# Kernel tuning notes

Measured on AMD Instinct MI355X. Metric: run time of the kernel, lower is better.

Reference implementation:

```python
import jax, jax.numpy as jnp
import numpy as np
import math

B, S, D, H = 2, 2048, 1024, 16
DK = D // H

def setup_inputs() -> dict:
    key = jax.random.key(0)
    ks = jax.random.split(key, 12)
    scale = 0.02
    return {
        "q": jax.random.normal(ks[0], (B, S, D), jnp.float32),
        "k": jax.random.normal(ks[1], (B, S, D), jnp.float32),
        "v": jax.random.normal(ks[2], (B, S, D), jnp.float32),
        "mask": jnp.ones((B, S), jnp.int32),
        "Wq": jax.random.normal(ks[3], (D, D), jnp.float32) * scale,
        "bq": jnp.zeros((D,), jnp.float32),
        "Wk": jax.random.normal(ks[4], (D, D), jnp.float32) * scale,
        "bk": jnp.zeros((D,), jnp.float32),
        "Wv": jax.random.normal(ks[5], (D, D), jnp.float32) * scale,
        "bv": jnp.zeros((D,), jnp.float32),
        "Wo": jax.random.normal(ks[6], (D, D), jnp.float32) * scale,
        "bo": jnp.zeros((D,), jnp.float32),
    }

def _split_heads(x):
    b, s, d = x.shape
    return x.reshape(b, s, H, DK).transpose(0, 2, 1, 3)  # [b,h,s,dk]

def reference(q, k, v, mask, Wq, bq, Wk, bk, Wv, bv, Wo, bo):
    Q = _split_heads(q @ Wq.T + bq)
    K = _split_heads(k @ Wk.T + bk)
    V = _split_heads(v @ Wv.T + bv)
    scores = jnp.einsum('bhqd,bhkd->bhqk', Q, K) / math.sqrt(DK)
    # mask dim==2 path: [b,s] -> [b,1,1,s]
    m = mask[:, None, None, :]
    scores = jnp.where(m == 0, jnp.float32(-1e9), scores)
    attn = jax.nn.softmax(scores, axis=-1)  # dropout is identity in eval
    out = jnp.einsum('bhqk,bhkd->bhqd', attn, V)
    out = out.transpose(0, 2, 1, 3).reshape(q.shape[0], q.shape[1], D)
    return out @ Wo.T + bo
```

## Files before the change

### kernel.cpp

```cpp
#include <hip/hip_runtime.h>
#include <math.h>

#define D_MODEL 1024
#define NHEAD   16
#define DKH     64
#define SEQ     2048
#define BATCH   2
#define TOK     (BATCH*SEQ)

typedef short s16x8 __attribute__((ext_vector_type(8)));
typedef float f32x4 __attribute__((ext_vector_type(4)));
typedef float f32x16 __attribute__((ext_vector_type(16)));
typedef unsigned short ushort_t;

__device__ inline unsigned short f2bf(float f) {
    union { float f; unsigned u; } v; v.f = f;
    unsigned r = v.u + 0x7FFFu + ((v.u >> 16) & 1u);
    return (unsigned short)(r >> 16);
}
__device__ inline float bf2f(ushort_t h) {
    union { unsigned u; float f; } v; v.u = (unsigned)h << 16;
    return v.f;
}
__device__ inline unsigned cvt_pk_bf16(float a, float b) {
    unsigned r;
    asm("v_cvt_pk_bf16_f32 %0, %1, %2" : "=v"(r) : "v"(a), "v"(b));
    return r;
}
__device__ inline void gload16(const void* g, void* l) {
    __builtin_amdgcn_global_load_lds(
        (const __attribute__((address_space(1))) void*)g,
        (__attribute__((address_space(3))) void*)l, 16, 0, 0);
}
__device__ inline f32x16 zero16() {
    f32x16 v;
#pragma unroll
    for (int i = 0; i < 16; ++i) v[i] = 0.f;
    return v;
}

__global__ __launch_bounds__(256) void convert_all(
    const float* __restrict__ q, const float* __restrict__ k,
    const float* __restrict__ v,
    const float* __restrict__ Wq, const float* __restrict__ Wk,
    const float* __restrict__ Wv, const float* __restrict__ Wo,
    const int* __restrict__ mask,
    ushort_t* __restrict__ qb, ushort_t* __restrict__ kb,
    ushort_t* __restrict__ vb,
    ushort_t* __restrict__ Wqb, ushort_t* __restrict__ Wkb,
    ushort_t* __restrict__ Wvb, ushort_t* __restrict__ Wohi,
    ushort_t* __restrict__ Wolo, float* __restrict__ mb)
{
    const int ACT4 = TOK * D_MODEL / 4;
    const int W4   = D_MODEL * D_MODEL / 4;
    const int total = 3 * ACT4 + 4 * W4 + TOK / 4;
    for (int u = blockIdx.x * 256 + threadIdx.x; u < total; u += gridDim.x * 256) {
        if (u < 3 * ACT4) {
            int which = u / ACT4, off = u - which * ACT4;
            const float* src = which == 0 ? q : which == 1 ? k : v;
            ushort_t*    dst = which == 0 ? qb : which == 1 ? kb : vb;
            float4 f = ((const float4*)src)[off];
            uint2 o;
            o.x = cvt_pk_bf16(f.x, f.y);
            o.y = cvt_pk_bf16(f.z, f.w);
            ((uint2*)dst)[off] = o;
        } else if (u < 3 * ACT4 + 3 * W4) {
            int uu = u - 3 * ACT4;
            int which = uu / W4, off = uu - which * W4;
            const float* src = which == 0 ? Wq : which == 1 ? Wk : Wv;
            ushort_t*    dst = which == 0 ? Wqb : which == 1 ? Wkb : Wvb;
            float4 f = ((const float4*)src)[off];
            uint2 o;
            o.x = cvt_pk_bf16(f.x, f.y);
            o.y = cvt_pk_bf16(f.z, f.w);
            ((uint2*)dst)[off] = o;
        } else if (u < 3 * ACT4 + 4 * W4) {
            int off = u - (3 * ACT4 + 3 * W4);
            float4 f = ((const float4*)Wo)[off];
            ushort_t h0 = f2bf(f.x), h1 = f2bf(f.y), h2 = f2bf(f.z), h3 = f2bf(f.w);
            uint2 hw;
            hw.x = (unsigned)h0 | ((unsigned)h1 << 16);
            hw.y = (unsigned)h2 | ((unsigned)h3 << 16);
            ((uint2*)Wohi)[off] = hw;
            uint2 lw;
            lw.x = cvt_pk_bf16(f.x - bf2f(h0), f.y - bf2f(h1));
            lw.y = cvt_pk_bf16(f.z - bf2f(h2), f.w - bf2f(h3));
            ((uint2*)Wolo)[off] = lw;
        } else {
            int off = u - (3 * ACT4 + 4 * W4);
            int4 m = ((const int4*)mask)[off];
            float4 f;
            f.x = m.x ? 0.f : -1e9f;
            f.y = m.y ? 0.f : -1e9f;
            f.z = m.z ? 0.f : -1e9f;
            f.w = m.w ? 0.f : -1e9f;
            ((float4*)mb)[off] = f;
        }
    }
}

__global__ __launch_bounds__(256) void gemm_qkv(
    const ushort_t* __restrict__ qb, const ushort_t* __restrict__ kb,
    const ushort_t* __restrict__ vb,
    const ushort_t* __restrict__ Wqb, const ushort_t* __restrict__ Wkb,
    const ushort_t* __restrict__ Wvb,
    const float* __restrict__ bqp, const float* __restrict__ bkp,
    const float* __restrict__ bvp,
    ushort_t* __restrict__ Qb, ushort_t* __restrict__ Kb,
    ushort_t* __restrict__ Vtb)
{
    __shared__ __align__(16) char pool[64 * 136 * 2];
    ushort_t* As = (ushort_t*)pool;
    ushort_t* Ws = As + 128 * 32;

    const int z = blockIdx.z;
    const ushort_t* Ain  = z == 0 ? qb : z == 1 ? kb : vb;
    const ushort_t* Wptr = z == 0 ? Wqb : z == 1 ? Wkb : Wvb;
    const float*    bias = z == 0 ? bqp : z == 1 ? bkp : bvp;

    const int hwid = blockIdx.x + 8 * blockIdx.y;
    const int work = (hwid & 7) * 32 + (hwid >> 3);
    const int m0 = (work >> 3) * 128;
    const int n0 = (work & 7) * 128;

    const int t = threadIdx.x;
    const int w = t >> 6, lane = t & 63, l15 = lane & 15, l4 = lane >> 4;
    const int wr = w >> 1, wc = w & 1;

    f32x4 acc[4][4];
#pragma unroll
    for (int m = 0; m < 4; ++m)
#pragma unroll
        for (int n = 0; n < 4; ++n) acc[m][n] = (f32x4){0.f, 0.f, 0.f, 0.f};

    const ushort_t* Ag = Ain  + (size_t)(m0 + (t >> 2)) * D_MODEL + (t & 3) * 8;
    const ushort_t* Wg = Wptr + (size_t)(n0 + (t >> 2)) * D_MODEL + (t & 3) * 8;
    ushort_t* AsW = As + w * 512;
    ushort_t* WsW = Ws + w * 512;

    for (int k0 = 0; k0 < D_MODEL; k0 += 32) {
        __syncthreads();
        gload16(Ag + k0, AsW);
        gload16(Ag + (size_t)64 * D_MODEL + k0, AsW + 2048);
        gload16(Wg + k0, WsW);
        gload16(Wg + (size_t)64 * D_MODEL + k0, WsW + 2048);
        __syncthreads();

        s16x8 af[4], bfr[4];
#pragma unroll
        for (int m = 0; m < 4; ++m)
            af[m] = *(const s16x8*)&As[(wr * 64 + m * 16 + l15) * 32 + l4 * 8];
#pragma unroll
        for (int n = 0; n < 4; ++n)
            bfr[n] = *(const s16x8*)&Ws[(wc * 64 + n * 16 + l15) * 32 + l4 * 8];
#pragma unroll
        for (int m = 0; m < 4; ++m)
#pragma unroll
            for (int n = 0; n < 4; ++n)
                acc[m][n] = __builtin_amdgcn_mfma_f32_16x16x32_bf16(af[m], bfr[n], acc[m][n], 0, 0, 0);
    }

    if (z == 2) {
        ushort_t* Ct = (ushort_t*)pool;
        const int h0 = n0 >> 6;
        const int bb = m0 >> 11;
        const int s0 = m0 & (SEQ - 1);
#pragma unroll
        for (int hh = 0; hh < 2; ++hh) {
            __syncthreads();
            if (wc == hh) {
#pragma unroll
                for (int n = 0; n < 4; ++n) {
                    const int nl = n * 16 + l15;
                    const float bv = bias[n0 + hh * 64 + nl];
#pragma unroll
                    for (int m = 0; m < 4; ++m) {
                        const int ml = wr * 64 + m * 16 + l4 * 4;
#pragma unroll
                        for (int r = 0; r < 4; ++r)
                            Ct[nl * 136 + ml + r] = f2bf(acc[m][n][r] + bv);
                    }
                }
            }
            __syncthreads();
            const int dl = t >> 2;
            ushort_t* dst = Vtb + (((size_t)bb * NHEAD + h0 + hh) * DKH + dl) * SEQ + s0;
#pragma unroll
            for (int c = 0; c < 4; ++c) {
                int chk = (t & 3) + c * 4;
                *(uint4*)&dst[chk * 8] = *(const uint4*)&Ct[dl * 136 + chk * 8];
            }
        }
    } else {
        ushort_t* Cout = z == 0 ? Qb : Kb;
#pragma unroll
        for (int n = 0; n < 4; ++n) {
            const int col = n0 + wc * 64 + n * 16 + l15;
            const float bv = bias[col];
#pragma unroll
            for (int m = 0; m < 4; ++m) {
                const int row = m0 + wr * 64 + m * 16 + l4 * 4;
#pragma unroll
                for (int r = 0; r < 4; ++r)
                    Cout[(size_t)(row + r) * D_MODEL + col] = f2bf(acc[m][n][r] + bv);
            }
        }
    }
}

__global__ __launch_bounds__(256) void gemm_out(
    const ushort_t* __restrict__ Ain, const ushort_t* __restrict__ Wptr,
    const ushort_t* __restrict__ W2ptr, const float* __restrict__ bias,
    float* __restrict__ Cout)
{
    __shared__ ushort_t As[128 * 32];
    __shared__ ushort_t Ws[64 * 32];
    __shared__ ushort_t Ws2[64 * 32];

    const int hwid = blockIdx.x + 16 * blockIdx.y;
    const int work = (hwid & 7) * 64 + (hwid >> 3);
    const int m0 = (work >> 4) * 128;
    const int n0 = (work & 15) * 64;

    const int t = threadIdx.x;
    const int w = t >> 6, lane = t & 63, l15 = lane & 15, l4 = lane >> 4;
    const int wr = w >> 1, wc = w & 1;

    f32x4 acc[4][2];
#pragma unroll
    for (int m = 0; m < 4; ++m)
#pragma unroll
        for (int n = 0; n < 2; ++n) acc[m][n] = (f32x4){0.f, 0.f, 0.f, 0.f};

    const ushort_t* Ag  = Ain   + (size_t)(m0 + (t >> 2)) * D_MODEL + (t & 3) * 8;
    const ushort_t* Wg  = Wptr  + (size_t)(n0 + (t >> 2)) * D_MODEL + (t & 3) * 8;
    const ushort_t* W2g = W2ptr + (size_t)(n0 + (t >> 2)) * D_MODEL + (t & 3) * 8;
    ushort_t* AsW = As + w * 512;
    ushort_t* WsW = Ws + w * 512;
    ushort_t* Ws2W = Ws2 + w * 512;

    for (int k0 = 0; k0 < D_MODEL; k0 += 32) {
        __syncthreads();
        gload16(Ag + k0, AsW);
        gload16(Ag + (size_t)64 * D_MODEL + k0, AsW + 2048);
        gload16(Wg + k0, WsW);
        gload16(W2g + k0, Ws2W);
        __syncthreads();

        s16x8 af[4], bfr[2], bfr2[2];
#pragma unroll
        for (int m = 0; m < 4; ++m)
            af[m] = *(const s16x8*)&As[(wr * 64 + m * 16 + l15) * 32 + l4 * 8];
#pragma unroll
        for (int n = 0; n < 2; ++n) {
            bfr[n]  = *(const s16x8*)&Ws[(wc * 32 + n * 16 + l15) * 32 + l4 * 8];
            bfr2[n] = *(const s16x8*)&Ws2[(wc * 32 + n * 16 + l15) * 32 + l4 * 8];
        }
#pragma unroll
        for (int m = 0; m < 4; ++m)
#pragma unroll
            for (int n = 0; n < 2; ++n) {
                acc[m][n] = __builtin_amdgcn_mfma_f32_16x16x32_bf16(af[m], bfr[n],  acc[m][n], 0, 0, 0);
                acc[m][n] = __builtin_amdgcn_mfma_f32_16x16x32_bf16(af[m], bfr2[n], acc[m][n], 0, 0, 0);
            }
    }

#pragma unroll
    for (int n = 0; n < 2; ++n) {
        const int col = n0 + wc * 32 + n * 16 + l15;
        const float bv = bias[col];
#pragma unroll
        for (int m = 0; m < 4; ++m) {
            const int row = m0 + wr * 64 + m * 16 + l4 * 4;
#pragma unroll
            for (int r = 0; r < 4; ++r)
                Cout[(size_t)(row + r) * D_MODEL + col] = acc[m][n][r] + bv;
        }
    }
}

__global__ __launch_bounds__(256) void flash5(
    const ushort_t* __restrict__ Q, const ushort_t* __restrict__ K,
    const ushort_t* __restrict__ Vt, const float* __restrict__ mb,
    ushort_t* __restrict__ Ctx)
{
    __shared__ ushort_t Ks[64 * 72];
    __shared__ ushort_t Vs[64 * 72];
    __shared__ ushort_t Ps[128 * 72];

    const int t = threadIdx.x;
    const int w = t >> 6, lane = t & 63;
    const int l31 = lane & 31, lh = lane >> 5;
    const int q0 = blockIdx.y * 128;
    const int bh = blockIdx.x, b = bh >> 4, h = bh & 15;

    s16x8 qf[4];
    {
        const ushort_t* qp = Q + ((size_t)b * SEQ + q0 + w * 32 + l31) * D_MODEL + h * DKH + lh * 8;
#pragma unroll
        for (int ks = 0; ks < 4; ++ks)
            qf[ks] = *(const s16x8*)(qp + ks * 16);
    }

    f32x16 oacc0 = zero16(), oacc1 = zero16();
    float lpart[16];
#pragma unroll
    for (int i = 0; i < 16; ++i) lpart[i] = 0.f;

    const int ch   = t & 7;
    const int row0 = t >> 3;
    const ushort_t* Kg = K  + ((size_t)b * SEQ) * D_MODEL + h * DKH + ch * 8;
    const ushort_t* Vg = Vt + ((size_t)bh * DKH) * SEQ + ch * 8;

    uint4 kr0 = *(const uint4*)&Kg[(size_t)row0 * D_MODEL];
    uint4 kr1 = *(const uint4*)&Kg[(size_t)(row0 + 32) * D_MODEL];
    uint4 vr0 = *(const uint4*)&Vg[(size_t)row0 * SEQ];
    uint4 vr1 = *(const uint4*)&Vg[(size_t)(row0 + 32) * SEQ];

    const float CSC = 0.18033688011112042f;
    const float* mbp = mb + b * SEQ;
    const int prow = w * 32;

    for (int k0 = 0; k0 < SEQ; k0 += 64) {
        __syncthreads();
        *(uint4*)&Ks[row0 * 72 + ch * 8]        = kr0;
        *(uint4*)&Ks[(row0 + 32) * 72 + ch * 8] = kr1;
        *(uint4*)&Vs[row0 * 72 + ch * 8]        = vr0;
        *(uint4*)&Vs[(row0 + 32) * 72 + ch * 8] = vr1;
        __syncthreads();
        if (k0 + 64 < SEQ) {
            kr0 = *(const uint4*)&Kg[(size_t)(k0 + 64 + row0) * D_MODEL];
            kr1 = *(const uint4*)&Kg[(size_t)(k0 + 64 + row0 + 32) * D_MODEL];
            vr0 = *(const uint4*)&Vg[(size_t)row0 * SEQ + k0 + 64];
            vr1 = *(const uint4*)&Vg[(size_t)(row0 + 32) * SEQ + k0 + 64];
        }
        const float mb0 = mbp[k0 + l31];
        const float mb1 = mbp[k0 + 32 + l31];

        f32x16 sacc0 = zero16(), sacc1 = zero16();
        __builtin_amdgcn_s_setprio(1);
#pragma unroll
        for (int ks = 0; ks < 4; ++ks) {
            s16x8 kf0 = *(const s16x8*)&Ks[(l31)      * 72 + ks * 16 + lh * 8];
            s16x8 kf1 = *(const s16x8*)&Ks[(32 + l31) * 72 + ks * 16 + lh * 8];
            sacc0 = __builtin_amdgcn_mfma_f32_32x32x16_bf16(qf[ks], kf0, sacc0, 0, 0, 0);
            sacc1 = __builtin_amdgcn_mfma_f32_32x32x16_bf16(qf[ks], kf1, sacc1, 0, 0, 0);
        }
        __builtin_amdgcn_s_setprio(0);

#pragma unroll
        for (int rp = 0; rp < 8; ++rp) {
            const int r0 = 2 * rp;
            const int rowb = (r0 & 3) + 8 * (r0 >> 2) + 4 * lh;
            float p0 = __builtin_amdgcn_exp2f(fmaf(sacc0[r0],     CSC, mb0));
            float p1 = __builtin_amdgcn_exp2f(fmaf(sacc0[r0 + 1], CSC, mb0));
            float p2 = __builtin_amdgcn_exp2f(fmaf(sacc1[r0],     CSC, mb1));
            float p3 = __builtin_amdgcn_exp2f(fmaf(sacc1[r0 + 1], CSC, mb1));
            lpart[r0]     += p0 + p2;
            lpart[r0 + 1] += p1 + p3;
            unsigned ua = cvt_pk_bf16(p0, p1);
            unsigned ub = cvt_pk_bf16(p2, p3);
            int base0 = (prow + rowb) * 72 + l31;
            Ps[base0]           = (ushort_t)ua;
            Ps[base0 + 72]      = (ushort_t)(ua >> 16);
            Ps[base0 + 32]      = (ushort_t)ub;
            Ps[base0 + 72 + 32] = (ushort_t)(ub >> 16);
        }
        __builtin_amdgcn_sched_barrier(0);

        __builtin_amdgcn_s_setprio(1);
#pragma unroll
        for (int ks = 0; ks < 4; ++ks) {
            s16x8 pa  = *(const s16x8*)&Ps[(prow + l31) * 72 + ks * 16 + lh * 8];
            s16x8 vf0 = *(const s16x8*)&Vs[(l31)      * 72 + ks * 16 + lh * 8];
            s16x8 vf1 = *(const s16x8*)&Vs[(32 + l31) * 72 + ks * 16 + lh * 8];
            oacc0 = __builtin_amdgcn_mfma_f32_32x32x16_bf16(pa, vf0, oacc0, 0, 0, 0);
            oacc1 = __builtin_amdgcn_mfma_f32_32x32x16_bf16(pa, vf1, oacc1, 0, 0, 0);
        }
        __builtin_amdgcn_s_setprio(0);
    }

#pragma unroll
    for (int rg = 0; rg < 16; ++rg) {
        lpart[rg] += __shfl_xor(lpart[rg], 1);
        lpart[rg] += __shfl_xor(lpart[rg], 2);
        lpart[rg] += __shfl_xor(lpart[rg], 4);
        lpart[rg] += __shfl_xor(lpart[rg], 8);
        lpart[rg] += __shfl_xor(lpart[rg], 16);
    }
    const size_t obase = ((size_t)b * SEQ + q0 + w * 32) * D_MODEL + h * DKH + l31;
#pragma unroll
    for (int rg = 0; rg < 16; ++rg) {
        const int qrow = (rg & 3) + 8 * (rg >> 2) + 4 * lh;
        const float inv = 1.f / lpart[rg];
        Ctx[obase + (size_t)qrow * D_MODEL]      = f2bf(oacc0[rg] * inv);
        Ctx[obase + (size_t)qrow * D_MODEL + 32] = f2bf(oacc1[rg] * inv);
    }
}

extern "C" void kernel_launch(void* const* d_in, const int* in_sizes, int n_in,
                              void* d_out, int out_size, void* d_ws, size_t ws_size,
                              hipStream_t stream) {
    const float* q    = (const float*)d_in[0];
    const float* k    = (const float*)d_in[1];
    const float* v    = (const float*)d_in[2];
    const int*   mask = (const int*)  d_in[3];
    const float* Wq   = (const float*)d_in[4];
    const float* bq   = (const float*)d_in[5];
    const float* Wk   = (const float*)d_in[6];
    const float* bk   = (const float*)d_in[7];
    const float* Wv   = (const float*)d_in[8];
    const float* bv   = (const float*)d_in[9];
    const float* Wo   = (const float*)d_in[10];
    const float* bo   = (const float*)d_in[11];
    float* out = (float*)d_out;

    char* ws = (char*)d_ws;
    ushort_t* Wqb  = (ushort_t*)(ws);
    ushort_t* Wkb  = (ushort_t*)(ws + ( 2u << 20));
    ushort_t* Wvb  = (ushort_t*)(ws + ( 4u << 20));
    ushort_t* Wohi = (ushort_t*)(ws + ( 6u << 20));
    ushort_t* Wolo = (ushort_t*)(ws + ( 8u << 20));
    float*    mb   = (float*)   (ws + (10u << 20));
    ushort_t* qb   = (ushort_t*)(ws + (12u << 20));
    ushort_t* kb   = (ushort_t*)(ws + (20u << 20));
    ushort_t* vb   = (ushort_t*)(ws + (28u << 20));
    ushort_t* Qb   = (ushort_t*)(ws + (36u << 20));
    ushort_t* Kb   = (ushort_t*)(ws + (44u << 20));
    ushort_t* Vtb  = (ushort_t*)(ws + (52u << 20));
    ushort_t* Ctx  = qb;

    convert_all<<<2048, 256, 0, stream>>>(q, k, v, Wq, Wk, Wv, Wo, mask,
                                          qb, kb, vb, Wqb, Wkb, Wvb,
                                          Wohi, Wolo, mb);

    dim3 qkvgrid(D_MODEL / 128, TOK / 128, 3);
    gemm_qkv<<<qkvgrid, 256, 0, stream>>>(qb, kb, vb, Wqb, Wkb, Wvb,
                                          bq, bk, bv, Qb, Kb, Vtb);

    dim3 agrid(BATCH * NHEAD, SEQ / 128);
    flash5<<<agrid, 256, 0, stream>>>(Qb, Kb, Vtb, mb, Ctx);

    dim3 ogrid(D_MODEL / 64, TOK / 128);
    gemm_out<<<ogrid, 256, 0, stream>>>(Ctx, Wohi, Wolo, bo, out);
}
```

Baseline: 150.6 us.

## Split attention over two key halves and add a combine kernel

The flash attention kernel now runs a third grid dimension that splits the key sequence into two halves. Each half writes unnormalized bf16 partial outputs and per-row softmax denominators to workspace, and a new combine kernel sums the two partials and normalizes them. This doubles the number of attention blocks, aiming to fill the GPU better than the previous 512-block grid. The cost is an extra launch, extra global traffic for two partial output buffers, and an added bf16 rounding of the unnormalized accumulators.

```diff
diff --git a/kernel.cpp b/kernel.cpp
--- a/kernel.cpp
+++ b/kernel.cpp
@@ -279,10 +279,11 @@
     }
 }
 
-__global__ __launch_bounds__(256) void flash5(
+__global__ __launch_bounds__(256) void flash8(
     const ushort_t* __restrict__ Q, const ushort_t* __restrict__ K,
     const ushort_t* __restrict__ Vt, const float* __restrict__ mb,
-    ushort_t* __restrict__ Ctx)
+    ushort_t* __restrict__ O0, ushort_t* __restrict__ O1,
+    float* __restrict__ Lp)
 {
     __shared__ ushort_t Ks[64 * 72];
     __shared__ ushort_t Vs[64 * 72];
@@ -293,6 +294,8 @@
     const int l31 = lane & 31, lh = lane >> 5;
     const int q0 = blockIdx.y * 128;
     const int bh = blockIdx.x, b = bh >> 4, h = bh & 15;
+    const int z  = blockIdx.z;
+    const int kbase = z * (SEQ / 2);
 
     s16x8 qf[4];
     {
@@ -312,23 +315,24 @@
     const ushort_t* Kg = K  + ((size_t)b * SEQ) * D_MODEL + h * DKH + ch * 8;
     const ushort_t* Vg = Vt + ((size_t)bh * DKH) * SEQ + ch * 8;
 
-    uint4 kr0 = *(const uint4*)&Kg[(size_t)row0 * D_MODEL];
-    uint4 kr1 = *(const uint4*)&Kg[(size_t)(row0 + 32) * D_MODEL];
-    uint4 vr0 = *(const uint4*)&Vg[(size_t)row0 * SEQ];
-    uint4 vr1 = *(const uint4*)&Vg[(size_t)(row0 + 32) * SEQ];
+    uint4 kr0 = *(const uint4*)&Kg[(size_t)(kbase + row0) * D_MODEL];
+    uint4 kr1 = *(const uint4*)&Kg[(size_t)(kbase + row0 + 32) * D_MODEL];
+    uint4 vr0 = *(const uint4*)&Vg[(size_t)row0 * SEQ + kbase];
+    uint4 vr1 = *(const uint4*)&Vg[(size_t)(row0 + 32) * SEQ + kbase];
 
     const float CSC = 0.18033688011112042f;
     const float* mbp = mb + b * SEQ;
     const int prow = w * 32;
 
-    for (int k0 = 0; k0 < SEQ; k0 += 64) {
+    const int kend = kbase + SEQ / 2;
+    for (int k0 = kbase; k0 < kend; k0 += 64) {
         __syncthreads();
         *(uint4*)&Ks[row0 * 72 + ch * 8]        = kr0;
         *(uint4*)&Ks[(row0 + 32) * 72 + ch * 8] = kr1;
         *(uint4*)&Vs[row0 * 72 + ch * 8]        = vr0;
         *(uint4*)&Vs[(row0 + 32) * 72 + ch * 8] = vr1;
         __syncthreads();
-        if (k0 + 64 < SEQ) {
+        if (k0 + 64 < kend) {
             kr0 = *(const uint4*)&Kg[(size_t)(k0 + 64 + row0) * D_MODEL];
             kr1 = *(const uint4*)&Kg[(size_t)(k0 + 64 + row0 + 32) * D_MODEL];
             vr0 = *(const uint4*)&Vg[(size_t)row0 * SEQ + k0 + 64];
@@ -388,14 +392,43 @@
         lpart[rg] += __shfl_xor(lpart[rg], 8);
         lpart[rg] += __shfl_xor(lpart[rg], 16);
     }
+    ushort_t* Op = z == 0 ? O0 : O1;
+    float* lp = Lp + (size_t)z * TOK * NHEAD;
     const size_t obase = ((size_t)b * SEQ + q0 + w * 32) * D_MODEL + h * DKH + l31;
 #pragma unroll
     for (int rg = 0; rg < 16; ++rg) {
         const int qrow = (rg & 3) + 8 * (rg >> 2) + 4 * lh;
-        const float inv = 1.f / lpart[rg];
-        Ctx[obase + (size_t)qrow * D_MODEL]      = f2bf(oacc0[rg] * inv);
-        Ctx[obase + (size_t)qrow * D_MODEL + 32] = f2bf(oacc1[rg] * inv);
-    }
+        Op[obase + (size_t)qrow * D_MODEL]      = f2bf(oacc0[rg]);
+        Op[obase + (size_t)qrow * D_MODEL + 32] = f2bf(oacc1[rg]);
+        if (l31 == 0)
+            lp[((size_t)b * SEQ + q0 + w * 32 + qrow) * NHEAD + h] = lpart[rg];
+    }
+}
+
+__global__ __launch_bounds__(256) void combine(
+    const ushort_t* __restrict__ O0, const ushort_t* __restrict__ O1,
+    const float* __restrict__ Lp, ushort_t* __restrict__ Ctx)
+{
+    const int idx = blockIdx.x * 256 + threadIdx.x;
+    const int e   = idx * 8;
+    const int row = e >> 10;
+    const int h   = (e & (D_MODEL - 1)) >> 6;
+    const float l0 = Lp[(size_t)row * NHEAD + h];
+    const float l1 = Lp[(size_t)TOK * NHEAD + (size_t)row * NHEAD + h];
+    const float inv = 1.f / (l0 + l1);
+    uint4 a = ((const uint4*)O0)[idx];
+    uint4 c = ((const uint4*)O1)[idx];
+    const unsigned* au = (const unsigned*)&a;
+    const unsigned* cu = (const unsigned*)&c;
+    uint4 o;
+    unsigned* ou = (unsigned*)&o;
+#pragma unroll
+    for (int j = 0; j < 4; ++j) {
+        float x0 = bf2f((ushort_t)(au[j] & 0xffff)) + bf2f((ushort_t)(cu[j] & 0xffff));
+        float x1 = bf2f((ushort_t)(au[j] >> 16))    + bf2f((ushort_t)(cu[j] >> 16));
+        ou[j] = cvt_pk_bf16(x0 * inv, x1 * inv);
+    }
+    ((uint4*)Ctx)[idx] = o;
 }
 
 extern "C" void kernel_launch(void* const* d_in, const int* in_sizes, int n_in,
@@ -422,6 +455,7 @@
     ushort_t* Wohi = (ushort_t*)(ws + ( 6u << 20));
     ushort_t* Wolo = (ushort_t*)(ws + ( 8u << 20));
     float*    mb   = (float*)   (ws + (10u << 20));
+    float*    Lp   = (float*)   (ws + (11u << 20));
     ushort_t* qb   = (ushort_t*)(ws + (12u << 20));
     ushort_t* kb   = (ushort_t*)(ws + (20u << 20));
     ushort_t* vb   = (ushort_t*)(ws + (28u << 20));
@@ -429,6 +463,8 @@
     ushort_t* Kb   = (ushort_t*)(ws + (44u << 20));
     ushort_t* Vtb  = (ushort_t*)(ws + (52u << 20));
     ushort_t* Ctx  = qb;
+    ushort_t* O0   = kb;
+    ushort_t* O1   = vb;
 
     convert_all<<<2048, 256, 0, stream>>>(q, k, v, Wq, Wk, Wv, Wo, mask,
                                           qb, kb, vb, Wqb, Wkb, Wvb,
@@ -438,8 +474,10 @@
     gemm_qkv<<<qkvgrid, 256, 0, stream>>>(qb, kb, vb, Wqb, Wkb, Wvb,
                                           bq, bk, bv, Qb, Kb, Vtb);
 
-    dim3 agrid(BATCH * NHEAD, SEQ / 128);
-    flash5<<<agrid, 256, 0, stream>>>(Qb, Kb, Vtb, mb, Ctx);
+    dim3 agrid(BATCH * NHEAD, SEQ / 128, 2);
+    flash8<<<agrid, 256, 0, stream>>>(Qb, Kb, Vtb, mb, O0, O1, Lp);
+
+    combine<<<TOK * D_MODEL / 8 / 256, 256, 0, stream>>>(O0, O1, Lp, Ctx);
 
     dim3 ogrid(D_MODEL / 64, TOK / 128);
     gemm_out<<<ogrid, 256, 0, stream>>>(Ctx, Wohi, Wolo, bo, out);
```

Result: slower. 155.5 us (+3.3%).
